# Kernel optimization log

Hardware: AMD Instinct MI355X
Metric: run time of the kernel (lower is better)

Reference implementation:

```python
import jax, jax.numpy as jnp
import numpy as np

N_NODES = 50000
N_EDGES = 1600000
IN_FEAT = 256
HID = IN_FEAT // 2  # 128
OUT_FEAT = 256


def setup_inputs() -> dict:
    key = jax.random.key(0)
    ks = jax.random.split(key, 10)
    x = jax.random.normal(ks[0], (N_NODES, IN_FEAT), dtype=jnp.float32)
    w = jax.random.uniform(ks[1], (N_EDGES, 1), dtype=jnp.float32)
    src = jax.random.randint(ks[2], (N_EDGES,), 0, N_NODES, dtype=jnp.int32)
    dst = jax.random.randint(ks[3], (N_EDGES,), 0, N_NODES, dtype=jnp.int32)
    s = 1.0 / np.sqrt(IN_FEAT)
    W_node = jax.random.uniform(ks[4], (IN_FEAT, HID), jnp.float32, -s, s)
    b_node = jax.random.uniform(ks[5], (HID,), jnp.float32, -s, s)
    W_edge = jax.random.uniform(ks[6], (IN_FEAT, HID), jnp.float32, -s, s)
    b_edge = jax.random.uniform(ks[7], (HID,), jnp.float32, -s, s)
    s2 = 1.0 / np.sqrt(HID)
    W_mlp = jax.random.uniform(ks[8], (HID, OUT_FEAT), jnp.float32, -s2, s2)
    b_mlp = jax.random.uniform(ks[9], (OUT_FEAT,), jnp.float32, -s2, s2)
    return {"x": x, "w": w, "src": src, "dst": dst,
            "W_node": W_node, "b_node": b_node,
            "W_edge": W_edge, "b_edge": b_edge,
            "W_mlp": W_mlp, "b_mlp": b_mlp}


def reference(x, w, src, dst, W_node, b_node, W_edge, b_edge, W_mlp, b_mlp):
    # message[v] = sum_{(u->v) in E} x[u] * w_e   (src_mul_edge + sum)
    message = jax.ops.segment_sum(x[src] * w, dst, num_segments=x.shape[0])  # [N, in_feat]
    h = (x @ W_node + b_node) + (message @ W_edge + b_edge)  # [N, in_feat//2]
    # NOTE: original uses nn.LeakyReLU(True) -> negative_slope=1.0 (identity);
    # replicated faithfully.
    h = jax.nn.leaky_relu(h, negative_slope=1.0)
    return h @ W_mlp + b_mlp  # [N, out_feat]
```

## Files before the change

kernel.cpp:

```cpp
#include <hip/hip_runtime.h>


constexpr int N_NODES  = 50000;
constexpr int N_EDGES  = 1600000;
constexpr int IN_FEAT  = 256;
constexpr int HID      = 128;
constexpr int OUT_FEAT = 256;

constexpr int BIN_SZ   = 32;
constexpr int N_BINS   = (N_NODES + BIN_SZ - 1) / BIN_SZ;
constexpr int CAPBIN   = 1536;
constexpr int EPB      = 4096;
constexpr int N_CBLK   = (N_EDGES + EPB - 1) / EPB;
constexpr int GRID_M   = (N_NODES + 127) / 128;
constexpr int N_G1BLK  = GRID_M * 2;

typedef __attribute__((ext_vector_type(8))) short bf16x8;
typedef __attribute__((ext_vector_type(8))) unsigned short u16x8;
typedef __attribute__((ext_vector_type(4))) float f32x4;

static __device__ __forceinline__ unsigned short f2bf(float f) {
    unsigned u = __builtin_bit_cast(unsigned, f);
    u += 0x7FFF + ((u >> 16) & 1);
    return (unsigned short)(u >> 16);
}
static __device__ __forceinline__ float bflo(unsigned u) {
    return __builtin_bit_cast(float, u << 16);
}
static __device__ __forceinline__ float bfhi(unsigned u) {
    return __builtin_bit_cast(float, u & 0xFFFF0000u);
}

__global__ __launch_bounds__(256) void k0_convert(
    const float* __restrict__ Wn, const float* __restrict__ We,
    const float* __restrict__ Wm,
    unsigned short* __restrict__ Wcat_t, unsigned short* __restrict__ Wmt)
{
    int n = blockIdx.x;
    int k = threadIdx.x;
    float v = (n < HID) ? Wn[(size_t)k * HID + n] : We[(size_t)k * HID + (n - HID)];
    Wcat_t[(size_t)n * IN_FEAT + k] = f2bf(v);
    if (k < HID) Wmt[(size_t)n * HID + k] = f2bf(Wm[(size_t)k * OUT_FEAT + n]);
}

union SharedU {
    struct {
        int  hist[N_BINS];
        int  gbase[N_BINS];
        int  wsum[8];
        int  stot;
        int2 sorted[EPB];
    } bc;
    struct {
        unsigned short As[128][64];
        unsigned short Bs[128][64];
    } g1;
};

__global__ __launch_bounds__(512, 4) void fuse1(
    const int* __restrict__ src, const int* __restrict__ dst,
    const float* __restrict__ w, int* __restrict__ cursor,
    int2* __restrict__ entries,
    const float* __restrict__ x, const unsigned short* __restrict__ Wcat_t,
    const float* __restrict__ bn, const float* __restrict__ be,
    float* __restrict__ h0, unsigned short* __restrict__ ybf)
{
    __shared__ SharedU sh;
    const int t = threadIdx.x;
    const int wave = t >> 6, lane = t & 63;
    const int r = blockIdx.x;

    if (r % 3 == 0) {
        const int e0 = (r / 3) * EPB;

        for (int i = t; i < N_BINS; i += 512) sh.bc.hist[i] = 0;
        __syncthreads();

        int meta[8], wb[8], rk[8], bin[8];
        #pragma unroll
        for (int k = 0; k < 8; ++k) {
            int e = e0 + t + k * 512;
            bin[k] = -1;
            if (e < N_EDGES) {
                int d = dst[e];
                int b = d >> 5;
                bin[k]  = b;
                meta[k] = src[e] | ((d & 31) << 16) | (b << 21);
                wb[k]   = __float_as_int(w[e]);
                rk[k]   = atomicAdd(&sh.bc.hist[b], 1);
            }
        }
        __syncthreads();

        const int b4 = t * 4;
        int c0 = 0, c1 = 0, c2 = 0, c3 = 0;
        if (b4 + 0 < N_BINS) c0 = sh.bc.hist[b4 + 0];
        if (b4 + 1 < N_BINS) c1 = sh.bc.hist[b4 + 1];
        if (b4 + 2 < N_BINS) c2 = sh.bc.hist[b4 + 2];
        if (b4 + 3 < N_BINS) c3 = sh.bc.hist[b4 + 3];
        const int s = c0 + c1 + c2 + c3;
        int pre = s;
        #pragma unroll
        for (int off = 1; off < 64; off <<= 1) {
            int o = __shfl_up(pre, off, 64);
            if (lane >= off) pre += o;
        }
        if (lane == 63) sh.bc.wsum[wave] = pre;
        __syncthreads();
        if (t == 0) {
            int rr = 0;
            #pragma unroll
            for (int q = 0; q < 8; ++q) { int v = sh.bc.wsum[q]; sh.bc.wsum[q] = rr; rr += v; }
            sh.bc.stot = rr;
        }
        __syncthreads();
        const int tb = sh.bc.wsum[wave] + pre - s;

        if (b4 + 0 < N_BINS) {
            sh.bc.hist[b4 + 0]  = tb;
            sh.bc.gbase[b4 + 0] = c0 ? atomicAdd(&cursor[b4 + 0], c0) : 0;
        }
        if (b4 + 1 < N_BINS) {
            sh.bc.hist[b4 + 1]  = tb + c0;
            sh.bc.gbase[b4 + 1] = c1 ? atomicAdd(&cursor[b4 + 1], c1) : 0;
        }
        if (b4 + 2 < N_BINS) {
            sh.bc.hist[b4 + 2]  = tb + c0 + c1;
            sh.bc.gbase[b4 + 2] = c2 ? atomicAdd(&cursor[b4 + 2], c2) : 0;
        }
        if (b4 + 3 < N_BINS) {
            sh.bc.hist[b4 + 3]  = tb + c0 + c1 + c2;
            sh.bc.gbase[b4 + 3] = c3 ? atomicAdd(&cursor[b4 + 3], c3) : 0;
        }
        __syncthreads();

        #pragma unroll
        for (int k = 0; k < 8; ++k)
            if (bin[k] >= 0)
                sh.bc.sorted[sh.bc.hist[bin[k]] + rk[k]] = make_int2(meta[k], wb[k]);
        __syncthreads();

        const int tot = sh.bc.stot;
        #pragma unroll
        for (int k = 0; k < 8; ++k) {
            int i = t + k * 512;
            if (i < tot) {
                int2 q = sh.bc.sorted[i];
                int b = ((unsigned)q.x) >> 21;
                int rr = i - sh.bc.hist[b];
                int g = sh.bc.gbase[b] + rr;
                if (g < CAPBIN)
                    entries[(size_t)b * CAPBIN + g] = make_int2(q.x & 0x1FFFFF, q.y);
            }
        }
    } else {
        const int bid2 = r - r / 3 - 1;
        const int m0 = (bid2 >> 1) * 128;
        const int nhalf = bid2 & 1;
        const int n0r = nhalf * 128;

        const int wm = wave >> 2, wn = wave & 3;
        const int la = lane & 15, kq = lane >> 4;
        const int srow = t >> 3, sc8 = t & 7;

        f32x4 acc[4][2];
        const f32x4 zero = {0.f, 0.f, 0.f, 0.f};
        #pragma unroll
        for (int i = 0; i < 4; ++i)
            #pragma unroll
            for (int j = 0; j < 2; ++j) acc[i][j] = zero;

        const float4* xg = (const float4*)x;

        for (int kt = 0; kt < 4; ++kt) {
            if (kt) __syncthreads();
            #pragma unroll
            for (int i = 0; i < 2; ++i) {
                int row = srow + i * 64;
                int node = m0 + row;
                float4 v0 = make_float4(0.f, 0.f, 0.f, 0.f), v1 = v0;
                if (node < N_NODES) {
                    v0 = xg[(size_t)node * 64 + kt * 16 + sc8 * 2];
                    v1 = xg[(size_t)node * 64 + kt * 16 + sc8 * 2 + 1];
                }
                u16x8 b;
                b[0] = f2bf(v0.x); b[1] = f2bf(v0.y); b[2] = f2bf(v0.z); b[3] = f2bf(v0.w);
                b[4] = f2bf(v1.x); b[5] = f2bf(v1.y); b[6] = f2bf(v1.z); b[7] = f2bf(v1.w);
                *(u16x8*)&sh.g1.As[row][(sc8 ^ (row & 7)) * 8] = b;
            }
            #pragma unroll
            for (int i = 0; i < 2; ++i) {
                int row = srow + i * 64;
                float4 v = *(const float4*)(
                    Wcat_t + (size_t)(n0r + row) * IN_FEAT + kt * 64 + sc8 * 8);
                *(float4*)&sh.g1.Bs[row][(sc8 ^ (row & 7)) * 8] = v;
            }
            __syncthreads();

            #pragma unroll
            for (int ks = 0; ks < 2; ++ks) {
                bf16x8 a[4], b[2];
                #pragma unroll
                for (int i = 0; i < 4; ++i) {
                    int row = wm * 64 + i * 16 + la;
                    a[i] = *(const bf16x8*)&sh.g1.As[row][((ks * 4 + kq) ^ (row & 7)) * 8];
                }
                #pragma unroll
                for (int j = 0; j < 2; ++j) {
                    int row = wn * 32 + j * 16 + la;
                    b[j] = *(const bf16x8*)&sh.g1.Bs[row][((ks * 4 + kq) ^ (row & 7)) * 8];
                }
                #pragma unroll
                for (int i = 0; i < 4; ++i)
                    #pragma unroll
                    for (int j = 0; j < 2; ++j)
                        acc[i][j] = __builtin_amdgcn_mfma_f32_16x16x32_bf16(
                            a[i], b[j], acc[i][j], 0, 0, 0);
            }
        }

        float bias[2];
        if (nhalf == 0) {
            #pragma unroll
            for (int j = 0; j < 2; ++j) {
                int n = wn * 32 + j * 16 + la;
                bias[j] = bn[n] + be[n];
            }
        }
        #pragma unroll
        for (int i = 0; i < 4; ++i) {
            int mbase = m0 + wm * 64 + i * 16 + kq * 4;
            #pragma unroll
            for (int j = 0; j < 2; ++j) {
                int n = wn * 32 + j * 16 + la;
                #pragma unroll
                for (int rr = 0; rr < 4; ++rr) {
                    int m = mbase + rr;
                    if (m < N_NODES) {
                        if (nhalf == 0)
                            h0[(size_t)m * HID + n] = acc[i][j][rr] + bias[j];
                        else
                            ybf[(size_t)m * HID + n] = f2bf(acc[i][j][rr]);
                    }
                }
            }
        }
    }
}

__global__ __launch_bounds__(512) void gatherB(
    const unsigned short* __restrict__ ybf, const float* __restrict__ h0,
    const int* __restrict__ cursor, const int2* __restrict__ entries,
    unsigned short* __restrict__ hbf)
{
    __shared__ int2 sorted[CAPBIN];
    __shared__ int  cnt32[BIN_SZ];
    __shared__ int  offs32[BIN_SZ];

    const int t = threadIdx.x;
    const int bin = blockIdx.x;
    const int node0 = bin * BIN_SZ;
    const int wave = t >> 6, lane = t & 63;

    const int tot = min(cursor[bin], CAPBIN);
    if (t < BIN_SZ) cnt32[t] = 0;
    __syncthreads();

    int2 held[3];
    int  hrank[3], hdloc[3];
    #pragma unroll
    for (int k = 0; k < 3; ++k) {
        hdloc[k] = -1;
        int g = t + k * 512;
        if (g < tot) {
            int2 ep = entries[(size_t)bin * CAPBIN + g];
            int dloc = ep.x >> 16;
            held[k]  = make_int2(ep.x & 0xFFFF, ep.y);
            hdloc[k] = dloc;
            hrank[k] = atomicAdd(&cnt32[dloc], 1);
        }
    }
    __syncthreads();

    if (wave == 0) {
        int v = (lane < BIN_SZ) ? cnt32[lane] : 0;
        int sum = v;
        #pragma unroll
        for (int off = 1; off < BIN_SZ; off <<= 1) {
            int o = __shfl_up(sum, off, 64);
            if (lane >= off) sum += o;
        }
        if (lane < BIN_SZ) offs32[lane] = sum - v;
    }
    __syncthreads();

    #pragma unroll
    for (int k = 0; k < 3; ++k)
        if (hdloc[k] >= 0)
            sorted[offs32[hdloc[k]] + hrank[k]] = held[k];
    __syncthreads();

    #pragma unroll
    for (int n4 = 0; n4 < 4; ++n4) {
        const int nl = wave * 4 + n4;
        const int node = node0 + nl;
        const int beg = offs32[nl];
        const int c = cnt32[nl];
        float a0 = 0.f, a1 = 0.f;
        int j = 0;
        for (; j + 4 <= c; j += 4) {
            int2 q0 = sorted[beg + j];
            int2 q1 = sorted[beg + j + 1];
            int2 q2 = sorted[beg + j + 2];
            int2 q3 = sorted[beg + j + 3];
            unsigned u0 = *(const unsigned*)&ybf[(size_t)q0.x * HID + 2 * lane];
            unsigned u1 = *(const unsigned*)&ybf[(size_t)q1.x * HID + 2 * lane];
            unsigned u2 = *(const unsigned*)&ybf[(size_t)q2.x * HID + 2 * lane];
            unsigned u3 = *(const unsigned*)&ybf[(size_t)q3.x * HID + 2 * lane];
            float w0 = __int_as_float(q0.y), w1 = __int_as_float(q1.y);
            float w2 = __int_as_float(q2.y), w3 = __int_as_float(q3.y);
            a0 += w0 * bflo(u0); a1 += w0 * bfhi(u0);
            a0 += w1 * bflo(u1); a1 += w1 * bfhi(u1);
            a0 += w2 * bflo(u2); a1 += w2 * bfhi(u2);
            a0 += w3 * bflo(u3); a1 += w3 * bfhi(u3);
        }
        for (; j < c; ++j) {
            int2 q = sorted[beg + j];
            unsigned u = *(const unsigned*)&ybf[(size_t)q.x * HID + 2 * lane];
            float wq = __int_as_float(q.y);
            a0 += wq * bflo(u); a1 += wq * bfhi(u);
        }
        if (node < N_NODES) {
            float2 hv = *(const float2*)&h0[(size_t)node * HID + 2 * lane];
            unsigned r = ((unsigned)f2bf(hv.y + a1) << 16)
                       | (unsigned)f2bf(hv.x + a0);
            *(unsigned*)&hbf[(size_t)node * HID + 2 * lane] = r;
        }
    }
}

__global__ __launch_bounds__(256, 4) void gemm2(
    const unsigned short* __restrict__ hbf, const unsigned short* __restrict__ Wmt,
    const float* __restrict__ bm, float* __restrict__ out)
{
    __shared__ unsigned short As[128][64];
    __shared__ unsigned short Bs[128][64];
    const int t = threadIdx.x;
    const int m0 = blockIdx.x * 128;
    const int n0 = blockIdx.y * 128;

    const int wave = t >> 6, lane = t & 63;
    const int wm = wave & 1, wn = wave >> 1;
    const int la = lane & 15, kq = lane >> 4;
    const int srow = t >> 3, sc8 = t & 7;

    f32x4 acc[4][4];
    const f32x4 zero = {0.f, 0.f, 0.f, 0.f};
    #pragma unroll
    for (int i = 0; i < 4; ++i)
        #pragma unroll
        for (int j = 0; j < 4; ++j) acc[i][j] = zero;

    for (int kt = 0; kt < 2; ++kt) {
        if (kt) __syncthreads();
        #pragma unroll
        for (int i = 0; i < 4; ++i) {
            int row = srow + i * 32;
            int node = m0 + row;
            if (node >= N_NODES) node = N_NODES - 1;
            float4 va = *(const float4*)(hbf + (size_t)node * HID + kt * 64 + sc8 * 8);
            float4 vb = *(const float4*)(Wmt + (size_t)(n0 + row) * HID + kt * 64 + sc8 * 8);
            *(float4*)&As[row][(sc8 ^ (row & 7)) * 8] = va;
            *(float4*)&Bs[row][(sc8 ^ (row & 7)) * 8] = vb;
        }
        __syncthreads();

        #pragma unroll
        for (int ks = 0; ks < 2; ++ks) {
            bf16x8 a[4], b[4];
            #pragma unroll
            for (int i = 0; i < 4; ++i) {
                int row = wm * 64 + i * 16 + la;
                a[i] = *(const bf16x8*)&As[row][((ks * 4 + kq) ^ (row & 7)) * 8];
            }
            #pragma unroll
            for (int j = 0; j < 4; ++j) {
                int row = wn * 64 + j * 16 + la;
                b[j] = *(const bf16x8*)&Bs[row][((ks * 4 + kq) ^ (row & 7)) * 8];
            }
            #pragma unroll
            for (int i = 0; i < 4; ++i)
                #pragma unroll
                for (int j = 0; j < 4; ++j)
                    acc[i][j] = __builtin_amdgcn_mfma_f32_16x16x32_bf16(
                        a[i], b[j], acc[i][j], 0, 0, 0);
        }
    }

    #pragma unroll
    for (int i = 0; i < 4; ++i) {
        int mbase = m0 + wm * 64 + i * 16 + kq * 4;
        #pragma unroll
        for (int j = 0; j < 4; ++j) {
            int n = n0 + wn * 64 + j * 16 + la;
            float b = bm[n];
            #pragma unroll
            for (int r = 0; r < 4; ++r) {
                int m = mbase + r;
                if (m < N_NODES)
                    out[(size_t)m * OUT_FEAT + n] = acc[i][j][r] + b;
            }
        }
    }
}

extern "C" void kernel_launch(void* const* d_in, const int* in_sizes, int n_in,
                              void* d_out, int out_size, void* d_ws, size_t ws_size,
                              hipStream_t stream) {
    const float* x   = (const float*)d_in[0];
    const float* w   = (const float*)d_in[1];
    const int*   src = (const int*)d_in[2];
    const int*   dst = (const int*)d_in[3];
    const float* Wn  = (const float*)d_in[4];
    const float* bn  = (const float*)d_in[5];
    const float* We  = (const float*)d_in[6];
    const float* be  = (const float*)d_in[7];
    const float* Wm  = (const float*)d_in[8];
    const float* bm  = (const float*)d_in[9];
    float* out = (float*)d_out;

    char* p = (char*)d_ws;
    float*          h0      = (float*)p;          p += (size_t)N_NODES * HID * 4;
    unsigned short* ybf     = (unsigned short*)p; p += (size_t)N_NODES * HID * 2;
    unsigned short* hbf     = (unsigned short*)p; p += (size_t)N_NODES * HID * 2;
    int2*           entries = (int2*)p;           p += (size_t)N_BINS * CAPBIN * 8;
    unsigned short* Wcat_t  = (unsigned short*)p; p += (size_t)256 * IN_FEAT * 2;
    unsigned short* Wmt     = (unsigned short*)p; p += (size_t)OUT_FEAT * HID * 2;
    int*            cursor  = (int*)p;            p += (size_t)N_BINS * 4;

    dim3 blk(256);

    hipMemsetAsync(cursor, 0, (size_t)N_BINS * 4, stream);
    k0_convert<<<256, blk, 0, stream>>>(Wn, We, Wm, Wcat_t, Wmt);
    fuse1<<<N_CBLK + N_G1BLK, dim3(512), 0, stream>>>(
        src, dst, w, cursor, entries, x, Wcat_t, bn, be, h0, ybf);
    gatherB<<<N_BINS, dim3(512), 0, stream>>>(ybf, h0, cursor, entries, hbf);
    gemm2<<<dim3(GRID_M, 2), blk, 0, stream>>>(hbf, Wmt, bm, out);
}
```

Measured before the change: 245.9 us.

## Sort bin edges by source-range and destination, gather per wave over merged node groups

The gather kernel now sorts each bin's edges by a combined key of source-node range (src>>13) and destination, instead of by destination alone. Each wave walks its four destination nodes together across the source-range buckets, with 8-wide unrolled loads and per-node accumulators picked by a branch on the destination. The aim is more concurrent ybf loads and better cache locality, since edges with nearby source rows are processed together across waves. The cost is a larger 256-entry histogram and scan, plus divergent select branches in the inner loop.

Result: slower. 254.9 us (+3.7%).

```diff
diff --git a/kernel.cpp b/kernel.cpp
--- a/kernel.cpp
+++ b/kernel.cpp
@@ -254,8 +254,8 @@
     unsigned short* __restrict__ hbf)
 {
     __shared__ int2 sorted[CAPBIN];
-    __shared__ int  cnt32[BIN_SZ];
-    __shared__ int  offs32[BIN_SZ];
+    __shared__ int  cnt[256];
+    __shared__ int  offs[256];
 
     const int t = threadIdx.x;
     const int bin = blockIdx.x;
@@ -263,73 +263,98 @@
     const int wave = t >> 6, lane = t & 63;
 
     const int tot = min(cursor[bin], CAPBIN);
-    if (t < BIN_SZ) cnt32[t] = 0;
+    if (t < 256) cnt[t] = 0;
     __syncthreads();
 
-    int2 held[3];
-    int  hrank[3], hdloc[3];
+    int  hx[3], hw[3], hkey[3], hrank[3];
     #pragma unroll
     for (int k = 0; k < 3; ++k) {
-        hdloc[k] = -1;
+        hkey[k] = -1;
         int g = t + k * 512;
         if (g < tot) {
             int2 ep = entries[(size_t)bin * CAPBIN + g];
             int dloc = ep.x >> 16;
-            held[k]  = make_int2(ep.x & 0xFFFF, ep.y);
-            hdloc[k] = dloc;
-            hrank[k] = atomicAdd(&cnt32[dloc], 1);
+            int srcq = (ep.x & 0xFFFF) >> 13;
+            int key  = srcq * 32 + dloc;
+            hx[k]    = ep.x;
+            hw[k]    = ep.y;
+            hkey[k]  = key;
+            hrank[k] = atomicAdd(&cnt[key], 1);
         }
     }
     __syncthreads();
 
     if (wave == 0) {
-        int v = (lane < BIN_SZ) ? cnt32[lane] : 0;
-        int sum = v;
-        #pragma unroll
-        for (int off = 1; off < BIN_SZ; off <<= 1) {
-            int o = __shfl_up(sum, off, 64);
-            if (lane >= off) sum += o;
-        }
-        if (lane < BIN_SZ) offs32[lane] = sum - v;
+        const int b4 = lane * 4;
+        int c0 = cnt[b4], c1 = cnt[b4 + 1], c2 = cnt[b4 + 2], c3 = cnt[b4 + 3];
+        const int s = c0 + c1 + c2 + c3;
+        int pre = s;
+        #pragma unroll
+        for (int off = 1; off < 64; off <<= 1) {
+            int o = __shfl_up(pre, off, 64);
+            if (lane >= off) pre += o;
+        }
+        const int tb = pre - s;
+        offs[b4 + 0] = tb;
+        offs[b4 + 1] = tb + c0;
+        offs[b4 + 2] = tb + c0 + c1;
+        offs[b4 + 3] = tb + c0 + c1 + c2;
     }
     __syncthreads();
 
     #pragma unroll
     for (int k = 0; k < 3; ++k)
-        if (hdloc[k] >= 0)
-            sorted[offs32[hdloc[k]] + hrank[k]] = held[k];
+        if (hkey[k] >= 0)
+            sorted[offs[hkey[k]] + hrank[k]] = make_int2(hx[k], hw[k]);
     __syncthreads();
+
+    const int w4 = wave * 4;
+    float s00 = 0.f, s01 = 0.f, s10 = 0.f, s11 = 0.f;
+    float s20 = 0.f, s21 = 0.f, s30 = 0.f, s31 = 0.f;
+
+    for (int q = 0; q < 7; ++q) {
+        const int beg = offs[q * 32 + w4];
+        const int end = (q * 32 + w4 + 4 < 256) ? offs[q * 32 + w4 + 4] : tot;
+        int j = beg;
+        for (; j + 8 <= end; j += 8) {
+            int2 e[8]; unsigned u[8];
+            #pragma unroll
+            for (int k = 0; k < 8; ++k) e[k] = sorted[j + k];
+            #pragma unroll
+            for (int k = 0; k < 8; ++k)
+                u[k] = *(const unsigned*)&ybf[(size_t)(e[k].x & 0xFFFF) * HID + 2 * lane];
+            #pragma unroll
+            for (int k = 0; k < 8; ++k) {
+                float wq = __int_as_float(e[k].y);
+                float lo = bflo(u[k]), hi = bfhi(u[k]);
+                int sel = (e[k].x >> 16) & 3;
+                if (sel == 0)      { s00 += wq * lo; s01 += wq * hi; }
+                else if (sel == 1) { s10 += wq * lo; s11 += wq * hi; }
+                else if (sel == 2) { s20 += wq * lo; s21 += wq * hi; }
+                else               { s30 += wq * lo; s31 += wq * hi; }
+            }
+        }
+        for (; j < end; ++j) {
+            int2 e = sorted[j];
+            unsigned u = *(const unsigned*)&ybf[(size_t)(e.x & 0xFFFF) * HID + 2 * lane];
+            float wq = __int_as_float(e.y);
+            float lo = bflo(u), hi = bfhi(u);
+            int sel = (e.x >> 16) & 3;
+            if (sel == 0)      { s00 += wq * lo; s01 += wq * hi; }
+            else if (sel == 1) { s10 += wq * lo; s11 += wq * hi; }
+            else if (sel == 2) { s20 += wq * lo; s21 += wq * hi; }
+            else               { s30 += wq * lo; s31 += wq * hi; }
+        }
+    }
 
     #pragma unroll
     for (int n4 = 0; n4 < 4; ++n4) {
-        const int nl = wave * 4 + n4;
-        const int node = node0 + nl;
-        const int beg = offs32[nl];
-        const int c = cnt32[nl];
-        float a0 = 0.f, a1 = 0.f;
-        int j = 0;
-        for (; j + 4 <= c; j += 4) {
-            int2 q0 = sorted[beg + j];
-            int2 q1 = sorted[beg + j + 1];
-            int2 q2 = sorted[beg + j + 2];
-            int2 q3 = sorted[beg + j + 3];
-            unsigned u0 = *(const unsigned*)&ybf[(size_t)q0.x * HID + 2 * lane];
-            unsigned u1 = *(const unsigned*)&ybf[(size_t)q1.x * HID + 2 * lane];
-            unsigned u2 = *(const unsigned*)&ybf[(size_t)q2.x * HID + 2 * lane];
-            unsigned u3 = *(const unsigned*)&ybf[(size_t)q3.x * HID + 2 * lane];
-            float w0 = __int_as_float(q0.y), w1 = __int_as_float(q1.y);
-            float w2 = __int_as_float(q2.y), w3 = __int_as_float(q3.y);
-            a0 += w0 * bflo(u0); a1 += w0 * bfhi(u0);
-            a0 += w1 * bflo(u1); a1 += w1 * bfhi(u1);
-            a0 += w2 * bflo(u2); a1 += w2 * bfhi(u2);
-            a0 += w3 * bflo(u3); a1 += w3 * bfhi(u3);
-        }
-        for (; j < c; ++j) {
-            int2 q = sorted[beg + j];
-            unsigned u = *(const unsigned*)&ybf[(size_t)q.x * HID + 2 * lane];
-            float wq = __int_as_float(q.y);
-            a0 += wq * bflo(u); a1 += wq * bfhi(u);
-        }
+        float a0, a1;
+        if (n4 == 0)      { a0 = s00; a1 = s01; }
+        else if (n4 == 1) { a0 = s10; a1 = s11; }
+        else if (n4 == 2) { a0 = s20; a1 = s21; }
+        else              { a0 = s30; a1 = s31; }
+        const int node = node0 + w4 + n4;
         if (node < N_NODES) {
             float2 hv = *(const float2*)&h0[(size_t)node * HID + 2 * lane];
             unsigned r = ((unsigned)f2bf(hv.y + a1) << 16)
```
